# Optimization experiments

Measured on AMD Instinct MI355X. Metric: run time of the kernel, lower is better.

Reference implementation:

```python
import jax, jax.numpy as jnp
import numpy as np

# config constants
H = 2048          # hidden_size
I_MOE = 1408      # moe_intermediate_size
E = 8             # n_routed_experts
TOP_K = 2         # num_experts_per_tok
NG = 4            # n_group
TOPK_G = 2        # topk_group
SCALE = 2.5       # routed_scaling_factor
N_SHARED = 2      # n_shared_experts
I_SHARED = I_MOE * N_SHARED
B, S = 1, 2048


def setup_inputs() -> dict:
    key = jax.random.key(0)
    ks = jax.random.split(key, 9)
    sc = 0.02
    return {
        "x": jax.random.normal(ks[0], (B, S, H), dtype=jnp.float32),
        "router_weight": jax.random.normal(ks[1], (E, H), dtype=jnp.float32) * sc,
        "e_score_correction_bias": jnp.zeros((E,), dtype=jnp.float32),
        "gate_w": jax.random.normal(ks[2], (E, I_MOE, H), dtype=jnp.float32) * sc,
        "up_w": jax.random.normal(ks[3], (E, I_MOE, H), dtype=jnp.float32) * sc,
        "down_w": jax.random.normal(ks[4], (E, H, I_MOE), dtype=jnp.float32) * sc,
        "shared_gate_w": jax.random.normal(ks[5], (I_SHARED, H), dtype=jnp.float32) * sc,
        "shared_up_w": jax.random.normal(ks[6], (I_SHARED, H), dtype=jnp.float32) * sc,
        "shared_down_w": jax.random.normal(ks[7], (H, I_SHARED), dtype=jnp.float32) * sc,
    }


def _mlp(x, gw, uw, dw):
    # SwiGLU MLP: down( silu(gate(x)) * up(x) )
    return (jax.nn.silu(x @ gw.T) * (x @ uw.T)) @ dw.T


def _route(x2d, rw, bias):
    T = x2d.shape[0]
    logits = x2d.astype(jnp.float32) @ rw.astype(jnp.float32).T          # [T,E]
    scores = jax.nn.sigmoid(logits)                                       # [T,E]
    sfc = scores + bias[None, :]                                          # [T,E]
    # group scores: sum of top-2 per group
    grp = sfc.reshape(T, NG, E // NG)
    group_scores = jnp.sum(jax.lax.top_k(grp, 2)[0], axis=-1)             # [T,NG]
    grp_idx = jax.lax.top_k(group_scores, TOPK_G)[1]                      # [T,topk_group]
    group_mask = jnp.zeros((T, NG), jnp.float32).at[
        jnp.arange(T)[:, None], grp_idx].set(1.0)                         # [T,NG]
    score_mask = jnp.repeat(group_mask, E // NG, axis=1)                  # [T,E]
    masked = jnp.where(score_mask > 0, sfc, 0.0)
    topk_idx = jax.lax.top_k(masked, TOP_K)[1]                            # [T,K]
    topk_w = jnp.take_along_axis(scores, topk_idx, axis=1)                # [T,K]
    topk_w = topk_w / (jnp.sum(topk_w, axis=-1, keepdims=True) + 1e-20)   # norm_topk_prob
    return topk_idx, topk_w * SCALE


def reference(x, router_weight, e_score_correction_bias, gate_w, up_w, down_w,
              shared_gate_w, shared_up_w, shared_down_w):
    orig_shape = x.shape
    x2d = x.reshape(-1, H)                                                # [T,H]
    T = x2d.shape[0]
    topk_idx, topk_w = _route(x2d, router_weight, e_score_correction_bias)
    # per-token per-expert combine weights [T,E] (top-k indices are distinct per token)
    cw = jnp.zeros((T, E), jnp.float32).at[
        jnp.arange(T)[:, None], topk_idx].add(topk_w)

    def expert_body(acc, ws):
        gw, uw, dw, cwe = ws  # gw/uw:[I,H], dw:[H,I], cwe:[T]
        y = _mlp(x2d, gw, uw, dw)
        return acc + cwe[:, None] * y, None

    routed, _ = jax.lax.scan(expert_body, jnp.zeros_like(x2d),
                             (gate_w, up_w, down_w, cw.T))
    out = routed.reshape(orig_shape) + _mlp(x, shared_gate_w, shared_up_w, shared_down_w)
    return out
```

## Files before the change

### kernel.cpp

```cpp
#include <hip/hip_runtime.h>
#include <hip/hip_bf16.h>
#include <math.h>

#define H 2048
#define IMOE 1408
#define NEXP 8
#define T_TOK 2048
#define ISH 2816
#define SCALEF 2.5f

#define NT_GU_R (IMOE / 64)
#define NT_GU_S (ISH / 64)
#define NT_DN   (H / 128)
#define GU_GRID (39 * NT_GU_R + 16 * NT_GU_S)
#define DN_GRID (39 * NT_DN + 16 * NT_DN)

typedef __attribute__((ext_vector_type(8))) short short8;
typedef __attribute__((ext_vector_type(4))) short short4v;
typedef __attribute__((ext_vector_type(4))) float floatx4;

union U8 { short8 s; unsigned u[4]; };

__device__ inline float b2f(short v) {
    unsigned int u = ((unsigned int)(unsigned short)v) << 16;
    float f; __builtin_memcpy(&f, &u, 4); return f;
}
__device__ inline short f2b(float f) {
    __hip_bfloat16 h = __float2bfloat16(f);
    short s; __builtin_memcpy(&s, &h, 2); return s;
}
__device__ __forceinline__ unsigned pkbf16(float a, float b) {
    float2 t; t.x = a; t.y = b;
    __hip_bfloat162 h2 = __float22bfloat162_rn(t);
    unsigned u; __builtin_memcpy(&u, &h2, 4); return u;
}

__device__ __forceinline__ void async16(const short* g, short* l) {
    __builtin_amdgcn_global_load_lds(
        (const __attribute__((address_space(1))) unsigned*)g,
        (__attribute__((address_space(3))) unsigned*)l, 16, 0, 0);
}

__global__ __launch_bounds__(256) void router_kernel(
    const float* __restrict__ x, const float* __restrict__ rw,
    const float* __restrict__ bias,
    int* __restrict__ cnt, int* __restrict__ tokList, int* __restrict__ slotList,
    float* __restrict__ pairW)
{
    const int wid  = (blockIdx.x * 256 + threadIdx.x) >> 6;
    const int lane = threadIdx.x & 63;
    if (wid >= T_TOK) return;
    const float* xr = x + (size_t)wid * H;

    float acc[NEXP];
#pragma unroll
    for (int e = 0; e < NEXP; ++e) acc[e] = 0.f;

#pragma unroll
    for (int c = 0; c < 8; ++c) {
        int idx = (c * 64 + lane) * 4;
        floatx4 xv = *(const floatx4*)(xr + idx);
#pragma unroll
        for (int e = 0; e < NEXP; ++e) {
            floatx4 wv = *(const floatx4*)(rw + e * H + idx);
            acc[e] += xv.x * wv.x + xv.y * wv.y + xv.z * wv.z + xv.w * wv.w;
        }
    }
#pragma unroll
    for (int e = 0; e < NEXP; ++e)
        for (int off = 32; off; off >>= 1)
            acc[e] += __shfl_xor(acc[e], off, 64);

    if (lane == 0) {
        float s[NEXP], sfc[NEXP];
#pragma unroll
        for (int e = 0; e < NEXP; ++e) {
            s[e]   = 1.0f / (1.0f + expf(-acc[e]));
            sfc[e] = s[e] + bias[e];
        }
        float gs[4];
#pragma unroll
        for (int g = 0; g < 4; ++g) gs[g] = sfc[2 * g] + sfc[2 * g + 1];
        int g1 = 0;
        for (int g = 1; g < 4; ++g) if (gs[g] > gs[g1]) g1 = g;
        int g2 = -1;
        for (int g = 0; g < 4; ++g) {
            if (g == g1) continue;
            if (g2 < 0 || gs[g] > gs[g2]) g2 = g;
        }
        float msk[NEXP];
#pragma unroll
        for (int e = 0; e < NEXP; ++e) {
            int g = e >> 1;
            msk[e] = (g == g1 || g == g2) ? sfc[e] : 0.0f;
        }
        int e1 = 0;
        for (int e = 1; e < NEXP; ++e) if (msk[e] > msk[e1]) e1 = e;
        int e2 = -1;
        for (int e = 0; e < NEXP; ++e) {
            if (e == e1) continue;
            if (e2 < 0 || msk[e] > msk[e2]) e2 = e;
        }
        float w1 = s[e1], w2 = s[e2];
        float inv = SCALEF / (w1 + w2 + 1e-20f);
        w1 *= inv; w2 *= inv;
        int p1 = atomicAdd(&cnt[e1], 1);
        tokList[e1 * T_TOK + p1]  = wid;
        slotList[e1 * T_TOK + p1] = 2 * wid;
        pairW[2 * wid] = w1;
        int p2 = atomicAdd(&cnt[e2], 1);
        tokList[e2 * T_TOK + p2]  = wid;
        slotList[e2 * T_TOK + p2] = 2 * wid + 1;
        pairW[2 * wid + 1] = w2;
    }
}

__global__ void plan_kernel(const int* __restrict__ cnt, int* __restrict__ meta)
{
    if (blockIdx.x != 0 || threadIdx.x != 0) return;
    int base = 0, gu = 0, dn = 0;
    meta[20] = 0; meta[32] = 0;
    for (int e = 0; e < NEXP; ++e) {
        int M = cnt[e];
        meta[e] = M;
        meta[9 + e] = base;
        base += M;
        int MT = (M + 127) >> 7;
        gu += MT * NT_GU_R;
        dn += MT * NT_DN;
        meta[21 + e] = gu;
        meta[33 + e] = dn;
    }
    meta[8]  = T_TOK;
    meta[17] = 0;
    meta[29] = gu + 16 * NT_GU_S;
    meta[41] = dn + 16 * NT_DN;
}

__global__ __launch_bounds__(256) void convert_kernel(
    const float* __restrict__ src, short* __restrict__ dst, int n4)
{
    int idx = blockIdx.x * 256 + threadIdx.x;
    int stride = gridDim.x * 256;
    for (; idx < n4; idx += stride) {
        floatx4 v = *(const floatx4*)(src + (size_t)idx * 4);
        short4v o = { f2b(v.x), f2b(v.y), f2b(v.z), f2b(v.w) };
        *(short4v*)(dst + (size_t)idx * 4) = o;
    }
}

__global__ __launch_bounds__(256) void gu_gemm(
    const short* __restrict__ xb,
    const float* __restrict__ gw, const float* __restrict__ uw,
    const float* __restrict__ sgw, const float* __restrict__ suw,
    short* __restrict__ hiddenP, short* __restrict__ hiddenS,
    const int* __restrict__ tokList, const int* __restrict__ meta)
{
    const int idx = blockIdx.x;
    if (idx >= meta[29]) return;
    int e = 0;
    while (e < 8 && idx >= meta[21 + e]) ++e;

    int M, NT, Nout, rowBase;
    const float *b1, *b2;
    const int* gat;
    short* outP;
    if (e < 8) {
        M = meta[e]; NT = NT_GU_R; Nout = IMOE; rowBase = meta[9 + e];
        b1 = gw + (size_t)e * IMOE * H;
        b2 = uw + (size_t)e * IMOE * H;
        gat = tokList + e * T_TOK;
        outP = hiddenP;
    } else {
        M = T_TOK; NT = NT_GU_S; Nout = ISH; rowBase = 0;
        b1 = sgw; b2 = suw; gat = nullptr; outP = hiddenS;
    }
    const int MT = (M + 127) >> 7;
    const int local = idx - meta[20 + e];
    const int mt = local % MT;
    const int nt = local / MT;

    __shared__ short As[128 * 64];
    __shared__ short Bg[64 * 64];
    __shared__ short Bu[64 * 64];

    const int tid  = threadIdx.x;
    const int w    = tid >> 6;
    const int lane = tid & 63;
    const int quad = lane >> 4;
    const int l16  = lane & 15;
    const int wm = w >> 1, wn = w & 1;

    const int r8 = lane >> 3;
    const int cs = (lane & 7) ^ r8;
    const short* aSrc[4];
    short* ldsA[4];
#pragma unroll
    for (int i = 0; i < 4; ++i) {
        int r = w * 32 + i * 8 + r8;
        int p = mt * 128 + r;
        int pos = p < M ? p : (M - 1);
        int arow = gat ? gat[pos] : pos;
        aSrc[i] = xb + (size_t)arow * H + cs * 8;
        ldsA[i] = As + (w * 32 + i * 8) * 64;
    }

    const int br = tid >> 2;
    const int bj = tid & 3;
    const int bs = br & 7;
    const float* b1p = b1 + (size_t)(nt * 64 + br) * H + bj * 16;
    const float* b2p = b2 + (size_t)(nt * 64 + br) * H + bj * 16;
    short* bgDst0 = Bg + br * 64 + (((2 * bj)    ) ^ bs) * 8;
    short* bgDst1 = Bg + br * 64 + (((2 * bj) + 1) ^ bs) * 8;
    short* buDst0 = Bu + br * 64 + (((2 * bj)    ) ^ bs) * 8;
    short* buDst1 = Bu + br * 64 + (((2 * bj) + 1) ^ bs) * 8;

    floatx4 accg[4][2] = {};
    floatx4 accu[4][2] = {};

    for (int k0 = 0; k0 < H; k0 += 64) {
#pragma unroll
        for (int i = 0; i < 4; ++i)
            async16(aSrc[i] + k0, ldsA[i]);
        {
            floatx4 v0 = ((const floatx4*)(b1p + k0))[0];
            floatx4 v1 = ((const floatx4*)(b1p + k0))[1];
            floatx4 v2 = ((const floatx4*)(b1p + k0))[2];
            floatx4 v3 = ((const floatx4*)(b1p + k0))[3];
            U8 lo, hi;
            lo.u[0] = pkbf16(v0.x, v0.y); lo.u[1] = pkbf16(v0.z, v0.w);
            lo.u[2] = pkbf16(v1.x, v1.y); lo.u[3] = pkbf16(v1.z, v1.w);
            hi.u[0] = pkbf16(v2.x, v2.y); hi.u[1] = pkbf16(v2.z, v2.w);
            hi.u[2] = pkbf16(v3.x, v3.y); hi.u[3] = pkbf16(v3.z, v3.w);
            *(short8*)bgDst0 = lo.s;
            *(short8*)bgDst1 = hi.s;
        }
        {
            floatx4 v0 = ((const floatx4*)(b2p + k0))[0];
            floatx4 v1 = ((const floatx4*)(b2p + k0))[1];
            floatx4 v2 = ((const floatx4*)(b2p + k0))[2];
            floatx4 v3 = ((const floatx4*)(b2p + k0))[3];
            U8 lo, hi;
            lo.u[0] = pkbf16(v0.x, v0.y); lo.u[1] = pkbf16(v0.z, v0.w);
            lo.u[2] = pkbf16(v1.x, v1.y); lo.u[3] = pkbf16(v1.z, v1.w);
            hi.u[0] = pkbf16(v2.x, v2.y); hi.u[1] = pkbf16(v2.z, v2.w);
            hi.u[2] = pkbf16(v3.x, v3.y); hi.u[3] = pkbf16(v3.z, v3.w);
            *(short8*)buDst0 = lo.s;
            *(short8*)buDst1 = hi.s;
        }
        __syncthreads();
        const int sw = l16 & 7;
        short8 af[4], bgf[2], buf[2];
#pragma unroll
        for (int kk2 = 0; kk2 < 2; ++kk2) {
            const int c = kk2 * 4 + quad;
#pragma unroll
            for (int m = 0; m < 4; ++m)
                af[m] = *(const short8*)(As + (wm * 64 + m * 16 + l16) * 64 + (c ^ sw) * 8);
#pragma unroll
            for (int n = 0; n < 2; ++n) {
                bgf[n] = *(const short8*)(Bg + (wn * 32 + n * 16 + l16) * 64 + (c ^ sw) * 8);
                buf[n] = *(const short8*)(Bu + (wn * 32 + n * 16 + l16) * 64 + (c ^ sw) * 8);
            }
#pragma unroll
            for (int m = 0; m < 4; ++m)
#pragma unroll
                for (int n = 0; n < 2; ++n) {
                    accg[m][n] = __builtin_amdgcn_mfma_f32_16x16x32_bf16(af[m], bgf[n], accg[m][n], 0, 0, 0);
                    accu[m][n] = __builtin_amdgcn_mfma_f32_16x16x32_bf16(af[m], buf[n], accu[m][n], 0, 0, 0);
                }
        }
        __syncthreads();
    }

#pragma unroll
    for (int m = 0; m < 4; ++m) {
#pragma unroll
        for (int rr = 0; rr < 4; ++rr) {
            int lr = wm * 64 + m * 16 + quad * 4 + rr;
            int p = mt * 128 + lr;
            if (p >= M) continue;
            size_t rowoff = (size_t)(rowBase + p) * Nout + nt * 64 + wn * 32;
#pragma unroll
            for (int n = 0; n < 2; ++n) {
                float g = accg[m][n][rr];
                float u = accu[m][n][rr];
                outP[rowoff + n * 16 + l16] = f2b(g / (1.0f + __expf(-g)) * u);
            }
        }
    }
}

__global__ __launch_bounds__(256) void dn_gemm(
    const short* __restrict__ hiddenP, const short* __restrict__ hiddenS,
    const float* __restrict__ dw, const float* __restrict__ sdw,
    short* __restrict__ outPairs, short* __restrict__ sharedOut,
    const int* __restrict__ slotList, const int* __restrict__ meta)
{
    const int idx = blockIdx.x;
    if (idx >= meta[41]) return;
    int e = 0;
    while (e < 8 && idx >= meta[33 + e]) ++e;

    int M, K, rowBase;
    const float* bp;
    const short* Abase;
    const int* scat;
    short* outP;
    if (e < 8) {
        M = meta[e]; K = IMOE; rowBase = meta[9 + e];
        bp = dw + (size_t)e * H * IMOE;
        Abase = hiddenP; scat = slotList + e * T_TOK; outP = outPairs;
    } else {
        M = T_TOK; K = ISH; rowBase = 0;
        bp = sdw; Abase = hiddenS; scat = nullptr; outP = sharedOut;
    }
    const int MT = (M + 127) >> 7;
    const int local = idx - meta[32 + e];
    const int mt = local % MT;
    const int nt = local / MT;

    __shared__ short As[128 * 64];
    __shared__ short Bs[128 * 64];

    const int tid  = threadIdx.x;
    const int w    = tid >> 6;
    const int lane = tid & 63;
    const int quad = lane >> 4;
    const int l16  = lane & 15;
    const int wm = w >> 1, wn = w & 1;

    const int r8 = lane >> 3;
    const int cs = (lane & 7) ^ r8;
    const short* aSrc[4];
    short* ldsA[4];
#pragma unroll
    for (int i = 0; i < 4; ++i) {
        int r = w * 32 + i * 8 + r8;
        int p = mt * 128 + r;
        int pos = p < M ? p : (M - 1);
        aSrc[i] = Abase + (size_t)(rowBase + pos) * K + cs * 8;
        ldsA[i] = As + (w * 32 + i * 8) * 64;
    }

    const int br = tid >> 1;
    const int bh = tid & 1;
    const int bs = br & 7;
    const float* bpp = bp + (size_t)(nt * 128 + br) * K + bh * 32;
    short* bDst[4];
#pragma unroll
    for (int i = 0; i < 4; ++i)
        bDst[i] = Bs + br * 64 + ((bh * 4 + i) ^ bs) * 8;

    floatx4 acc[4][4] = {};

    const int kIters = K >> 6;
    for (int kt = 0; kt < kIters; ++kt) {
        const int k0 = kt << 6;
#pragma unroll
        for (int i = 0; i < 4; ++i)
            async16(aSrc[i] + k0, ldsA[i]);
#pragma unroll
        for (int i = 0; i < 4; ++i) {
            floatx4 v0 = ((const floatx4*)(bpp + k0))[2 * i];
            floatx4 v1 = ((const floatx4*)(bpp + k0))[2 * i + 1];
            U8 c;
            c.u[0] = pkbf16(v0.x, v0.y); c.u[1] = pkbf16(v0.z, v0.w);
            c.u[2] = pkbf16(v1.x, v1.y); c.u[3] = pkbf16(v1.z, v1.w);
            *(short8*)bDst[i] = c.s;
        }
        __syncthreads();
        const int sw = l16 & 7;
        short8 af[4], bf[4];
#pragma unroll
        for (int kk2 = 0; kk2 < 2; ++kk2) {
            const int c = kk2 * 4 + quad;
#pragma unroll
            for (int m = 0; m < 4; ++m)
                af[m] = *(const short8*)(As + (wm * 64 + m * 16 + l16) * 64 + (c ^ sw) * 8);
#pragma unroll
            for (int n = 0; n < 4; ++n)
                bf[n] = *(const short8*)(Bs + (wn * 64 + n * 16 + l16) * 64 + (c ^ sw) * 8);
#pragma unroll
            for (int m = 0; m < 4; ++m)
#pragma unroll
                for (int n = 0; n < 4; ++n)
                    acc[m][n] = __builtin_amdgcn_mfma_f32_16x16x32_bf16(af[m], bf[n], acc[m][n], 0, 0, 0);
        }
        __syncthreads();
    }

#pragma unroll
    for (int m = 0; m < 4; ++m) {
#pragma unroll
        for (int rr = 0; rr < 4; ++rr) {
            int lr = wm * 64 + m * 16 + quad * 4 + rr;
            int p = mt * 128 + lr;
            if (p >= M) continue;
            int crow = scat ? scat[p] : p;
            size_t rowoff = (size_t)crow * H + nt * 128 + wn * 64;
#pragma unroll
            for (int n = 0; n < 4; ++n)
                outP[rowoff + n * 16 + l16] = f2b(acc[m][n][rr]);
        }
    }
}

__global__ __launch_bounds__(256) void combine_kernel(
    const short* __restrict__ outPairs, const short* __restrict__ sharedOut,
    const float* __restrict__ pairW, float* __restrict__ out)
{
    size_t gi = ((size_t)blockIdx.x * 256 + threadIdx.x) * 8;
    int t = (int)(gi >> 11);
    int h = (int)(gi & (H - 1));
    float w0 = pairW[2 * t], w1 = pairW[2 * t + 1];
    short8 p0 = *(const short8*)(outPairs + (size_t)(2 * t) * H + h);
    short8 p1 = *(const short8*)(outPairs + (size_t)(2 * t + 1) * H + h);
    short8 sh = *(const short8*)(sharedOut + gi);
    floatx4 o0, o1;
#pragma unroll
    for (int j = 0; j < 4; ++j)
        o0[j] = w0 * b2f(p0[j]) + w1 * b2f(p1[j]) + b2f(sh[j]);
#pragma unroll
    for (int j = 0; j < 4; ++j)
        o1[j] = w0 * b2f(p0[4 + j]) + w1 * b2f(p1[4 + j]) + b2f(sh[4 + j]);
    *(floatx4*)(out + gi)     = o0;
    *(floatx4*)(out + gi + 4) = o1;
}

extern "C" void kernel_launch(void* const* d_in, const int* in_sizes, int n_in,
                              void* d_out, int out_size, void* d_ws, size_t ws_size,
                              hipStream_t stream)
{
    const float* x    = (const float*)d_in[0];
    const float* rw   = (const float*)d_in[1];
    const float* bias = (const float*)d_in[2];
    const float* gw   = (const float*)d_in[3];
    const float* uw   = (const float*)d_in[4];
    const float* dw   = (const float*)d_in[5];
    const float* sgw  = (const float*)d_in[6];
    const float* suw  = (const float*)d_in[7];
    const float* sdw  = (const float*)d_in[8];
    float* out = (float*)d_out;

    char* ws = (char*)d_ws;
    size_t off = 0;
    auto alloc = [&](size_t bytes) {
        off = (off + 255) & ~(size_t)255;
        void* p = ws + off;
        off += bytes;
        return p;
    };
    int*   cnt       = (int*)  alloc(NEXP * sizeof(int));
    int*   tokList   = (int*)  alloc((size_t)NEXP * T_TOK * sizeof(int));
    int*   slotList  = (int*)  alloc((size_t)NEXP * T_TOK * sizeof(int));
    float* pairW     = (float*)alloc((size_t)2 * T_TOK * sizeof(float));
    int*   meta      = (int*)  alloc(64 * sizeof(int));
    short* xb        = (short*)alloc((size_t)T_TOK * H * sizeof(short));
    short* hiddenP   = (short*)alloc((size_t)2 * T_TOK * IMOE * sizeof(short));
    short* hiddenS   = (short*)alloc((size_t)T_TOK * ISH * sizeof(short));
    short* outPairs  = (short*)alloc((size_t)2 * T_TOK * H * sizeof(short));
    short* sharedOut = (short*)alloc((size_t)T_TOK * H * sizeof(short));
    (void)ws_size;

    hipMemsetAsync(cnt, 0, NEXP * sizeof(int), stream);

    router_kernel<<<T_TOK / 4, 256, 0, stream>>>(x, rw, bias, cnt, tokList, slotList, pairW);
    plan_kernel<<<1, 64, 0, stream>>>(cnt, meta);
    convert_kernel<<<2048, 256, 0, stream>>>(x, xb, T_TOK * H / 4);

    gu_gemm<<<GU_GRID, 256, 0, stream>>>(xb, gw, uw, sgw, suw,
                                         hiddenP, hiddenS, tokList, meta);
    dn_gemm<<<DN_GRID, 256, 0, stream>>>(hiddenP, hiddenS, dw, sdw,
                                         outPairs, sharedOut, slotList, meta);

    combine_kernel<<<(T_TOK * H / 8) / 256, 256, 0, stream>>>(outPairs, sharedOut, pairW, out);
}
```

Baseline: 700.9 us.

## Pre-convert weights to bf16 buffers and schedule GEMM tiles per XCD

Adds separate conversion passes that turn the fp32 expert and shared weights into bf16 workspace buffers. The GEMMs then load B tiles with async global-to-LDS copies instead of converting fp32 to bf16 in registers inside the loop. The fp32 path remains as a fallback when the workspace is too small. The plan kernel also builds per-XCD tile tables with greedy load balancing, so blocks with the same blockIdx mod 8 share weight tiles. The cost is an extra full read and write of every weight each call, in exchange for half-size, reused bf16 reads in the GEMMs.

```diff
diff --git a/kernel.cpp b/kernel.cpp
--- a/kernel.cpp
+++ b/kernel.cpp
@@ -12,8 +12,8 @@
 #define NT_GU_R (IMOE / 64)
 #define NT_GU_S (ISH / 64)
 #define NT_DN   (H / 128)
-#define GU_GRID (39 * NT_GU_R + 16 * NT_GU_S)
-#define DN_GRID (39 * NT_DN + 16 * NT_DN)
+#define XCAP_GU 224
+#define XCAP_DN 136
 
 typedef __attribute__((ext_vector_type(8))) short short8;
 typedef __attribute__((ext_vector_type(4))) short short4v;
@@ -34,7 +34,6 @@
     __hip_bfloat162 h2 = __float22bfloat162_rn(t);
     unsigned u; __builtin_memcpy(&u, &h2, 4); return u;
 }
-
 __device__ __forceinline__ void async16(const short* g, short* l) {
     __builtin_amdgcn_global_load_lds(
         (const __attribute__((address_space(1))) unsigned*)g,
@@ -115,26 +114,38 @@
     }
 }
 
-__global__ void plan_kernel(const int* __restrict__ cnt, int* __restrict__ meta)
-{
-    if (blockIdx.x != 0 || threadIdx.x != 0) return;
-    int base = 0, gu = 0, dn = 0;
-    meta[20] = 0; meta[32] = 0;
+__global__ void plan_kernel(const int* __restrict__ cnt, int* __restrict__ meta,
+                            int* __restrict__ guTab, int* __restrict__ dnTab)
+{
+    if (threadIdx.x != 0 || blockIdx.x != 0) return;
+    int base = 0;
     for (int e = 0; e < NEXP; ++e) {
-        int M = cnt[e];
-        meta[e] = M;
+        meta[e] = cnt[e];
         meta[9 + e] = base;
-        base += M;
+        base += cnt[e];
+    }
+    meta[8] = T_TOK;
+    meta[17] = 0;
+    int loadG[8] = {0,0,0,0,0,0,0,0};
+    int loadD[8] = {0,0,0,0,0,0,0,0};
+    for (int ent = 0; ent < 9; ++ent) {
+        int M  = (ent < 8) ? cnt[ent] : T_TOK;
         int MT = (M + 127) >> 7;
-        gu += MT * NT_GU_R;
-        dn += MT * NT_DN;
-        meta[21 + e] = gu;
-        meta[33 + e] = dn;
-    }
-    meta[8]  = T_TOK;
-    meta[17] = 0;
-    meta[29] = gu + 16 * NT_GU_S;
-    meta[41] = dn + 16 * NT_DN;
+        int NT = (ent < 8) ? NT_GU_R : NT_GU_S;
+        for (int nt = 0; nt < NT; ++nt) {
+            int c = 0;
+            for (int j = 1; j < 8; ++j) if (loadG[j] < loadG[c]) c = j;
+            for (int mt = 0; mt < MT; ++mt)
+                guTab[c * XCAP_GU + loadG[c]++] = (ent << 16) | (nt << 8) | mt;
+        }
+        for (int nt = 0; nt < NT_DN; ++nt) {
+            int c = 0;
+            for (int j = 1; j < 8; ++j) if (loadD[j] < loadD[c]) c = j;
+            for (int mt = 0; mt < MT; ++mt)
+                dnTab[c * XCAP_DN + loadD[c]++] = (ent << 16) | (nt << 8) | mt;
+        }
+    }
+    for (int c = 0; c < 8; ++c) { meta[44 + c] = loadG[c]; meta[52 + c] = loadD[c]; }
 }
 
 __global__ __launch_bounds__(256) void convert_kernel(
@@ -151,34 +162,39 @@
 
 __global__ __launch_bounds__(256) void gu_gemm(
     const short* __restrict__ xb,
+    const short* __restrict__ gwb, const short* __restrict__ uwb,
     const float* __restrict__ gw, const float* __restrict__ uw,
+    const short* __restrict__ sgwb, const short* __restrict__ suwb,
     const float* __restrict__ sgw, const float* __restrict__ suw,
     short* __restrict__ hiddenP, short* __restrict__ hiddenS,
-    const int* __restrict__ tokList, const int* __restrict__ meta)
-{
-    const int idx = blockIdx.x;
-    if (idx >= meta[29]) return;
-    int e = 0;
-    while (e < 8 && idx >= meta[21 + e]) ++e;
-
-    int M, NT, Nout, rowBase;
-    const float *b1, *b2;
+    const int* __restrict__ tokList, const int* __restrict__ meta,
+    const int* __restrict__ guTab)
+{
+    const int c8 = blockIdx.x & 7;
+    const int ti = blockIdx.x >> 3;
+    if (ti >= meta[44 + c8]) return;
+    const int t = guTab[c8 * XCAP_GU + ti];
+    const int e = t >> 16, nt = (t >> 8) & 255, mt = t & 255;
+
+    int M, Nout, rowBase;
+    const short *bg16, *bu16;
+    const float *bg32, *bu32;
     const int* gat;
     short* outP;
     if (e < 8) {
-        M = meta[e]; NT = NT_GU_R; Nout = IMOE; rowBase = meta[9 + e];
-        b1 = gw + (size_t)e * IMOE * H;
-        b2 = uw + (size_t)e * IMOE * H;
+        M = meta[e]; Nout = IMOE; rowBase = meta[9 + e];
+        bg16 = gwb ? gwb + (size_t)e * IMOE * H : nullptr;
+        bu16 = uwb ? uwb + (size_t)e * IMOE * H : nullptr;
+        bg32 = gw + (size_t)e * IMOE * H;
+        bu32 = uw + (size_t)e * IMOE * H;
         gat = tokList + e * T_TOK;
         outP = hiddenP;
     } else {
-        M = T_TOK; NT = NT_GU_S; Nout = ISH; rowBase = 0;
-        b1 = sgw; b2 = suw; gat = nullptr; outP = hiddenS;
-    }
-    const int MT = (M + 127) >> 7;
-    const int local = idx - meta[20 + e];
-    const int mt = local % MT;
-    const int nt = local / MT;
+        M = T_TOK; Nout = ISH; rowBase = 0;
+        bg16 = sgwb; bu16 = suwb; bg32 = sgw; bu32 = suw;
+        gat = nullptr; outP = hiddenS;
+    }
+    const bool useB16 = (bg16 != nullptr);
 
     __shared__ short As[128 * 64];
     __shared__ short Bg[64 * 64];
@@ -193,6 +209,7 @@
 
     const int r8 = lane >> 3;
     const int cs = (lane & 7) ^ r8;
+
     const short* aSrc[4];
     short* ldsA[4];
 #pragma unroll
@@ -205,62 +222,22 @@
         ldsA[i] = As + (w * 32 + i * 8) * 64;
     }
 
-    const int br = tid >> 2;
-    const int bj = tid & 3;
-    const int bs = br & 7;
-    const float* b1p = b1 + (size_t)(nt * 64 + br) * H + bj * 16;
-    const float* b2p = b2 + (size_t)(nt * 64 + br) * H + bj * 16;
-    short* bgDst0 = Bg + br * 64 + (((2 * bj)    ) ^ bs) * 8;
-    short* bgDst1 = Bg + br * 64 + (((2 * bj) + 1) ^ bs) * 8;
-    short* buDst0 = Bu + br * 64 + (((2 * bj)    ) ^ bs) * 8;
-    short* buDst1 = Bu + br * 64 + (((2 * bj) + 1) ^ bs) * 8;
-
     floatx4 accg[4][2] = {};
     floatx4 accu[4][2] = {};
 
-    for (int k0 = 0; k0 < H; k0 += 64) {
-#pragma unroll
-        for (int i = 0; i < 4; ++i)
-            async16(aSrc[i] + k0, ldsA[i]);
-        {
-            floatx4 v0 = ((const floatx4*)(b1p + k0))[0];
-            floatx4 v1 = ((const floatx4*)(b1p + k0))[1];
-            floatx4 v2 = ((const floatx4*)(b1p + k0))[2];
-            floatx4 v3 = ((const floatx4*)(b1p + k0))[3];
-            U8 lo, hi;
-            lo.u[0] = pkbf16(v0.x, v0.y); lo.u[1] = pkbf16(v0.z, v0.w);
-            lo.u[2] = pkbf16(v1.x, v1.y); lo.u[3] = pkbf16(v1.z, v1.w);
-            hi.u[0] = pkbf16(v2.x, v2.y); hi.u[1] = pkbf16(v2.z, v2.w);
-            hi.u[2] = pkbf16(v3.x, v3.y); hi.u[3] = pkbf16(v3.z, v3.w);
-            *(short8*)bgDst0 = lo.s;
-            *(short8*)bgDst1 = hi.s;
-        }
-        {
-            floatx4 v0 = ((const floatx4*)(b2p + k0))[0];
-            floatx4 v1 = ((const floatx4*)(b2p + k0))[1];
-            floatx4 v2 = ((const floatx4*)(b2p + k0))[2];
-            floatx4 v3 = ((const floatx4*)(b2p + k0))[3];
-            U8 lo, hi;
-            lo.u[0] = pkbf16(v0.x, v0.y); lo.u[1] = pkbf16(v0.z, v0.w);
-            lo.u[2] = pkbf16(v1.x, v1.y); lo.u[3] = pkbf16(v1.z, v1.w);
-            hi.u[0] = pkbf16(v2.x, v2.y); hi.u[1] = pkbf16(v2.z, v2.w);
-            hi.u[2] = pkbf16(v3.x, v3.y); hi.u[3] = pkbf16(v3.z, v3.w);
-            *(short8*)buDst0 = lo.s;
-            *(short8*)buDst1 = hi.s;
-        }
-        __syncthreads();
+    auto mfma_step = [&]() {
         const int sw = l16 & 7;
         short8 af[4], bgf[2], buf[2];
 #pragma unroll
         for (int kk2 = 0; kk2 < 2; ++kk2) {
-            const int c = kk2 * 4 + quad;
+            const int cc = kk2 * 4 + quad;
 #pragma unroll
             for (int m = 0; m < 4; ++m)
-                af[m] = *(const short8*)(As + (wm * 64 + m * 16 + l16) * 64 + (c ^ sw) * 8);
+                af[m] = *(const short8*)(As + (wm * 64 + m * 16 + l16) * 64 + (cc ^ sw) * 8);
 #pragma unroll
             for (int n = 0; n < 2; ++n) {
-                bgf[n] = *(const short8*)(Bg + (wn * 32 + n * 16 + l16) * 64 + (c ^ sw) * 8);
-                buf[n] = *(const short8*)(Bu + (wn * 32 + n * 16 + l16) * 64 + (c ^ sw) * 8);
+                bgf[n] = *(const short8*)(Bg + (wn * 32 + n * 16 + l16) * 64 + (cc ^ sw) * 8);
+                buf[n] = *(const short8*)(Bu + (wn * 32 + n * 16 + l16) * 64 + (cc ^ sw) * 8);
             }
 #pragma unroll
             for (int m = 0; m < 4; ++m)
@@ -270,7 +247,76 @@
                     accu[m][n] = __builtin_amdgcn_mfma_f32_16x16x32_bf16(af[m], buf[n], accu[m][n], 0, 0, 0);
                 }
         }
-        __syncthreads();
+    };
+
+    if (useB16) {
+        const short* bgSrc[2];
+        const short* buSrc[2];
+        short* ldsBg[2];
+        short* ldsBu[2];
+#pragma unroll
+        for (int i = 0; i < 2; ++i) {
+            int r = w * 16 + i * 8 + r8;
+            bgSrc[i] = bg16 + (size_t)(nt * 64 + r) * H + cs * 8;
+            buSrc[i] = bu16 + (size_t)(nt * 64 + r) * H + cs * 8;
+            ldsBg[i] = Bg + (w * 16 + i * 8) * 64;
+            ldsBu[i] = Bu + (w * 16 + i * 8) * 64;
+        }
+        for (int k0 = 0; k0 < H; k0 += 64) {
+#pragma unroll
+            for (int i = 0; i < 4; ++i) async16(aSrc[i] + k0, ldsA[i]);
+#pragma unroll
+            for (int i = 0; i < 2; ++i) {
+                async16(bgSrc[i] + k0, ldsBg[i]);
+                async16(buSrc[i] + k0, ldsBu[i]);
+            }
+            __syncthreads();
+            mfma_step();
+            __syncthreads();
+        }
+    } else {
+        const int br = tid >> 2;
+        const int bj = tid & 3;
+        const int bs = br & 7;
+        const float* b1p = bg32 + (size_t)(nt * 64 + br) * H + bj * 16;
+        const float* b2p = bu32 + (size_t)(nt * 64 + br) * H + bj * 16;
+        short* bgDst0 = Bg + br * 64 + (((2 * bj)    ) ^ bs) * 8;
+        short* bgDst1 = Bg + br * 64 + (((2 * bj) + 1) ^ bs) * 8;
+        short* buDst0 = Bu + br * 64 + (((2 * bj)    ) ^ bs) * 8;
+        short* buDst1 = Bu + br * 64 + (((2 * bj) + 1) ^ bs) * 8;
+        for (int k0 = 0; k0 < H; k0 += 64) {
+#pragma unroll
+            for (int i = 0; i < 4; ++i) async16(aSrc[i] + k0, ldsA[i]);
+            {
+                floatx4 v0 = ((const floatx4*)(b1p + k0))[0];
+                floatx4 v1 = ((const floatx4*)(b1p + k0))[1];
+                floatx4 v2 = ((const floatx4*)(b1p + k0))[2];
+                floatx4 v3 = ((const floatx4*)(b1p + k0))[3];
+                U8 lo, hi;
+                lo.u[0] = pkbf16(v0.x, v0.y); lo.u[1] = pkbf16(v0.z, v0.w);
+                lo.u[2] = pkbf16(v1.x, v1.y); lo.u[3] = pkbf16(v1.z, v1.w);
+                hi.u[0] = pkbf16(v2.x, v2.y); hi.u[1] = pkbf16(v2.z, v2.w);
+                hi.u[2] = pkbf16(v3.x, v3.y); hi.u[3] = pkbf16(v3.z, v3.w);
+                *(short8*)bgDst0 = lo.s;
+                *(short8*)bgDst1 = hi.s;
+            }
+            {
+                floatx4 v0 = ((const floatx4*)(b2p + k0))[0];
+                floatx4 v1 = ((const floatx4*)(b2p + k0))[1];
+                floatx4 v2 = ((const floatx4*)(b2p + k0))[2];
+                floatx4 v3 = ((const floatx4*)(b2p + k0))[3];
+                U8 lo, hi;
+                lo.u[0] = pkbf16(v0.x, v0.y); lo.u[1] = pkbf16(v0.z, v0.w);
+                lo.u[2] = pkbf16(v1.x, v1.y); lo.u[3] = pkbf16(v1.z, v1.w);
+                hi.u[0] = pkbf16(v2.x, v2.y); hi.u[1] = pkbf16(v2.z, v2.w);
+                hi.u[2] = pkbf16(v3.x, v3.y); hi.u[3] = pkbf16(v3.z, v3.w);
+                *(short8*)buDst0 = lo.s;
+                *(short8*)buDst1 = hi.s;
+            }
+            __syncthreads();
+            mfma_step();
+            __syncthreads();
+        }
     }
 
 #pragma unroll
@@ -293,32 +339,35 @@
 
 __global__ __launch_bounds__(256) void dn_gemm(
     const short* __restrict__ hiddenP, const short* __restrict__ hiddenS,
+    const short* __restrict__ dwb, const short* __restrict__ sdwb,
     const float* __restrict__ dw, const float* __restrict__ sdw,
     short* __restrict__ outPairs, short* __restrict__ sharedOut,
-    const int* __restrict__ slotList, const int* __restrict__ meta)
-{
-    const int idx = blockIdx.x;
-    if (idx >= meta[41]) return;
-    int e = 0;
-    while (e < 8 && idx >= meta[33 + e]) ++e;
+    const int* __restrict__ slotList, const int* __restrict__ meta,
+    const int* __restrict__ dnTab)
+{
+    const int c8 = blockIdx.x & 7;
+    const int ti = blockIdx.x >> 3;
+    if (ti >= meta[52 + c8]) return;
+    const int t = dnTab[c8 * XCAP_DN + ti];
+    const int e = t >> 16, nt = (t >> 8) & 255, mt = t & 255;
 
     int M, K, rowBase;
-    const float* bp;
+    const short* b16;
+    const float* b32;
     const short* Abase;
     const int* scat;
     short* outP;
     if (e < 8) {
         M = meta[e]; K = IMOE; rowBase = meta[9 + e];
-        bp = dw + (size_t)e * H * IMOE;
+        b16 = dwb ? dwb + (size_t)e * H * IMOE : nullptr;
+        b32 = dw + (size_t)e * H * IMOE;
         Abase = hiddenP; scat = slotList + e * T_TOK; outP = outPairs;
     } else {
         M = T_TOK; K = ISH; rowBase = 0;
-        bp = sdw; Abase = hiddenS; scat = nullptr; outP = sharedOut;
-    }
-    const int MT = (M + 127) >> 7;
-    const int local = idx - meta[32 + e];
-    const int mt = local % MT;
-    const int nt = local / MT;
+        b16 = sdwb; b32 = sdw;
+        Abase = hiddenS; scat = nullptr; outP = sharedOut;
+    }
+    const bool useB16 = (b16 != nullptr);
 
     __shared__ short As[128 * 64];
     __shared__ short Bs[128 * 64];
@@ -332,6 +381,7 @@
 
     const int r8 = lane >> 3;
     const int cs = (lane & 7) ^ r8;
+
     const short* aSrc[4];
     short* ldsA[4];
 #pragma unroll
@@ -343,51 +393,71 @@
         ldsA[i] = As + (w * 32 + i * 8) * 64;
     }
 
-    const int br = tid >> 1;
-    const int bh = tid & 1;
-    const int bs = br & 7;
-    const float* bpp = bp + (size_t)(nt * 128 + br) * K + bh * 32;
-    short* bDst[4];
-#pragma unroll
-    for (int i = 0; i < 4; ++i)
-        bDst[i] = Bs + br * 64 + ((bh * 4 + i) ^ bs) * 8;
-
     floatx4 acc[4][4] = {};
 
-    const int kIters = K >> 6;
-    for (int kt = 0; kt < kIters; ++kt) {
-        const int k0 = kt << 6;
-#pragma unroll
-        for (int i = 0; i < 4; ++i)
-            async16(aSrc[i] + k0, ldsA[i]);
-#pragma unroll
-        for (int i = 0; i < 4; ++i) {
-            floatx4 v0 = ((const floatx4*)(bpp + k0))[2 * i];
-            floatx4 v1 = ((const floatx4*)(bpp + k0))[2 * i + 1];
-            U8 c;
-            c.u[0] = pkbf16(v0.x, v0.y); c.u[1] = pkbf16(v0.z, v0.w);
-            c.u[2] = pkbf16(v1.x, v1.y); c.u[3] = pkbf16(v1.z, v1.w);
-            *(short8*)bDst[i] = c.s;
-        }
-        __syncthreads();
+    auto mfma_step = [&]() {
         const int sw = l16 & 7;
         short8 af[4], bf[4];
 #pragma unroll
         for (int kk2 = 0; kk2 < 2; ++kk2) {
-            const int c = kk2 * 4 + quad;
+            const int cc = kk2 * 4 + quad;
 #pragma unroll
             for (int m = 0; m < 4; ++m)
-                af[m] = *(const short8*)(As + (wm * 64 + m * 16 + l16) * 64 + (c ^ sw) * 8);
+                af[m] = *(const short8*)(As + (wm * 64 + m * 16 + l16) * 64 + (cc ^ sw) * 8);
 #pragma unroll
             for (int n = 0; n < 4; ++n)
-                bf[n] = *(const short8*)(Bs + (wn * 64 + n * 16 + l16) * 64 + (c ^ sw) * 8);
+                bf[n] = *(const short8*)(Bs + (wn * 64 + n * 16 + l16) * 64 + (cc ^ sw) * 8);
 #pragma unroll
             for (int m = 0; m < 4; ++m)
 #pragma unroll
                 for (int n = 0; n < 4; ++n)
                     acc[m][n] = __builtin_amdgcn_mfma_f32_16x16x32_bf16(af[m], bf[n], acc[m][n], 0, 0, 0);
         }
-        __syncthreads();
+    };
+
+    if (useB16) {
+        const short* bSrc[4];
+        short* ldsB[4];
+#pragma unroll
+        for (int i = 0; i < 4; ++i) {
+            int r = w * 32 + i * 8 + r8;
+            bSrc[i] = b16 + (size_t)(nt * 128 + r) * K + cs * 8;
+            ldsB[i] = Bs + (w * 32 + i * 8) * 64;
+        }
+        for (int k0 = 0; k0 < K; k0 += 64) {
+#pragma unroll
+            for (int i = 0; i < 4; ++i) async16(aSrc[i] + k0, ldsA[i]);
+#pragma unroll
+            for (int i = 0; i < 4; ++i) async16(bSrc[i] + k0, ldsB[i]);
+            __syncthreads();
+            mfma_step();
+            __syncthreads();
+        }
+    } else {
+        const int br = tid >> 1;
+        const int bh = tid & 1;
+        const int bs = br & 7;
+        const float* bpp = b32 + (size_t)(nt * 128 + br) * K + bh * 32;
+        short* bDst[4];
+#pragma unroll
+        for (int i = 0; i < 4; ++i)
+            bDst[i] = Bs + br * 64 + ((bh * 4 + i) ^ bs) * 8;
+        for (int k0 = 0; k0 < K; k0 += 64) {
+#pragma unroll
+            for (int i = 0; i < 4; ++i) async16(aSrc[i] + k0, ldsA[i]);
+#pragma unroll
+            for (int i = 0; i < 4; ++i) {
+                floatx4 v0 = ((const floatx4*)(bpp + k0))[2 * i];
+                floatx4 v1 = ((const floatx4*)(bpp + k0))[2 * i + 1];
+                U8 cv;
+                cv.u[0] = pkbf16(v0.x, v0.y); cv.u[1] = pkbf16(v0.z, v0.w);
+                cv.u[2] = pkbf16(v1.x, v1.y); cv.u[3] = pkbf16(v1.z, v1.w);
+                *(short8*)bDst[i] = cv.s;
+            }
+            __syncthreads();
+            mfma_step();
+            __syncthreads();
+        }
     }
 
 #pragma unroll
@@ -451,28 +521,57 @@
         off += bytes;
         return p;
     };
-    int*   cnt       = (int*)  alloc(NEXP * sizeof(int));
-    int*   tokList   = (int*)  alloc((size_t)NEXP * T_TOK * sizeof(int));
-    int*   slotList  = (int*)  alloc((size_t)NEXP * T_TOK * sizeof(int));
-    float* pairW     = (float*)alloc((size_t)2 * T_TOK * sizeof(float));
-    int*   meta      = (int*)  alloc(64 * sizeof(int));
-    short* xb        = (short*)alloc((size_t)T_TOK * H * sizeof(short));
-    short* hiddenP   = (short*)alloc((size_t)2 * T_TOK * IMOE * sizeof(short));
-    short* hiddenS   = (short*)alloc((size_t)T_TOK * ISH * sizeof(short));
-    short* outPairs  = (short*)alloc((size_t)2 * T_TOK * H * sizeof(short));
-    short* sharedOut = (short*)alloc((size_t)T_TOK * H * sizeof(short));
-    (void)ws_size;
+    int*   cnt      = (int*)  alloc(NEXP * sizeof(int));
+    int*   tokList  = (int*)  alloc((size_t)NEXP * T_TOK * sizeof(int));
+    int*   slotList = (int*)  alloc((size_t)NEXP * T_TOK * sizeof(int));
+    float* pairW    = (float*)alloc((size_t)2 * T_TOK * sizeof(float));
+    int*   meta     = (int*)  alloc(64 * sizeof(int));
+    int*   guTab    = (int*)  alloc((size_t)8 * XCAP_GU * sizeof(int));
+    int*   dnTab    = (int*)  alloc((size_t)8 * XCAP_DN * sizeof(int));
+    short* xb       = (short*)alloc((size_t)T_TOK * H * sizeof(short));
+    short* hiddenP  = (short*)alloc((size_t)2 * T_TOK * IMOE * sizeof(short));
+    short* hiddenS  = (short*)alloc((size_t)T_TOK * ISH * sizeof(short));
+    short* A1 = (short*)alloc((size_t)NEXP * IMOE * H * sizeof(short));
+    short* A2 = (short*)alloc((size_t)NEXP * IMOE * H * sizeof(short));
+    size_t off_tierR = off;
+    short* A3 = (short*)alloc((size_t)ISH * H * sizeof(short));
+    short* A4 = (short*)alloc((size_t)ISH * H * sizeof(short));
+    size_t off_tierS = off;
+
+    int tier = (ws_size >= off_tierS) ? 2 : (ws_size >= off_tierR) ? 1 : 0;
+
+    short* outPairs  = (tier >= 1) ? A2 : A1;
+    short* sharedOut = outPairs + (size_t)2 * T_TOK * H;
 
     hipMemsetAsync(cnt, 0, NEXP * sizeof(int), stream);
-
     router_kernel<<<T_TOK / 4, 256, 0, stream>>>(x, rw, bias, cnt, tokList, slotList, pairW);
-    plan_kernel<<<1, 64, 0, stream>>>(cnt, meta);
+    plan_kernel<<<1, 64, 0, stream>>>(cnt, meta, guTab, dnTab);
     convert_kernel<<<2048, 256, 0, stream>>>(x, xb, T_TOK * H / 4);
 
-    gu_gemm<<<GU_GRID, 256, 0, stream>>>(xb, gw, uw, sgw, suw,
-                                         hiddenP, hiddenS, tokList, meta);
-    dn_gemm<<<DN_GRID, 256, 0, stream>>>(hiddenP, hiddenS, dw, sdw,
-                                         outPairs, sharedOut, slotList, meta);
+    if (tier >= 1) {
+        convert_kernel<<<2048, 256, 0, stream>>>(gw, A1, NEXP * IMOE * H / 4);
+        convert_kernel<<<2048, 256, 0, stream>>>(uw, A2, NEXP * IMOE * H / 4);
+    }
+    if (tier >= 2) {
+        convert_kernel<<<2048, 256, 0, stream>>>(sgw, A3, ISH * H / 4);
+        convert_kernel<<<2048, 256, 0, stream>>>(suw, A4, ISH * H / 4);
+    }
+
+    gu_gemm<<<8 * XCAP_GU, 256, 0, stream>>>(
+        xb,
+        (tier >= 1) ? A1 : nullptr, (tier >= 1) ? A2 : nullptr, gw, uw,
+        (tier >= 2) ? A3 : nullptr, (tier >= 2) ? A4 : nullptr, sgw, suw,
+        hiddenP, hiddenS, tokList, meta, guTab);
+
+    if (tier >= 1)
+        convert_kernel<<<2048, 256, 0, stream>>>(dw, A1, NEXP * H * IMOE / 4);
+    if (tier >= 2)
+        convert_kernel<<<2048, 256, 0, stream>>>(sdw, A3, H * ISH / 4);
+
+    dn_gemm<<<8 * XCAP_DN, 256, 0, stream>>>(
+        hiddenP, hiddenS,
+        (tier >= 1) ? A1 : nullptr, (tier >= 2) ? A3 : nullptr, dw, sdw,
+        outPairs, sharedOut, slotList, meta, dnTab);
 
     combine_kernel<<<(T_TOK * H / 8) / 256, 256, 0, stream>>>(outPairs, sharedOut, pairW, out);
 }
```

Result: slower. 919.1 us (+31.1%).
